# Performance work log

Hardware: AMD Instinct MI355X
Metric: run time of the kernel (lower is better)

The kernel has to match this reference:

```python
import jax, jax.numpy as jnp
import numpy as np

E, B, C_IN, H, W = 4, 32, 64, 64, 64
C_OUT, KH, KW = 128, 3, 3


def setup_inputs() -> dict:
    key = jax.random.key(0)
    k1, k2 = jax.random.split(key)
    features = jax.random.normal(k1, (E, B, C_IN, H, W), dtype=jnp.float32)
    # weight: ensemble + (in, out) + kernel, Glorot-style std = out_channels**-0.5
    weight = jax.random.normal(k2, (E, C_IN, C_OUT, KH, KW), dtype=jnp.float32) * (C_OUT ** -0.5)
    bias = jnp.zeros((E, C_OUT), dtype=jnp.float32)
    return {"features": features, "weight": weight, "bias": bias}


def reference(features, weight, bias):
    # features: (E, B, C_in, H, W); weight: (E, C_in, C_out, KH, KW); bias: (E, C_out)
    # The torch module's unfold+einsum equals a VALID cross-correlation per ensemble member:
    # out[e,b,j,y,x] = sum_{i,A,B} features[e,b,i,y+A,x+B] * weight[e,i,j,A,B]
    def conv_one(x, w):
        k = jnp.transpose(w, (1, 0, 2, 3))  # (C_out, C_in, KH, KW) = OIHW
        return jax.lax.conv_general_dilated(
            x, k, window_strides=(1, 1), padding="VALID",
            dimension_numbers=("NCHW", "OIHW", "NCHW"))

    out = jax.vmap(conv_one)(features, weight)  # (E, B, C_out, H', W')
    out = out + bias[:, None, :, None, None]
    return out
```

## Files before the change

### kernel.cpp

```cpp
#include <hip/hip_runtime.h>

typedef __bf16 bf16x8 __attribute__((ext_vector_type(8)));
typedef __bf16 bf16x2 __attribute__((ext_vector_type(2)));
typedef float  f32x4  __attribute__((ext_vector_type(4)));

#define FT_BYTES 67108864ull

__device__ __forceinline__ void gl2lds16(const void* g, void* l) {
    __builtin_amdgcn_global_load_lds(
        (const __attribute__((address_space(1))) void*)g,
        (__attribute__((address_space(3))) void*)l, 16, 0, 0);
}

__global__ void wt_prep(const float* __restrict__ w, __bf16* __restrict__ wt) {
    int o = blockIdx.x * 256 + threadIdx.x;
    int i = o & 63, j = (o >> 6) & 127, et = o >> 13;
    int tap = et % 9, e = et / 9;
    wt[o] = (__bf16)w[((e * 64 + i) * 128 + j) * 9 + tap];
}

__global__ void ft_prep(const float* __restrict__ f, __bf16* __restrict__ ft) {
    __shared__ float s[64 * 65];
    int eb = blockIdx.z * 32 + blockIdx.y, y = blockIdx.x;
    const float* src = f + (size_t)eb * 262144 + y * 64;
    int t = threadIdx.x;
    for (int r = 0; r < 4; ++r) {
        int f4 = r * 256 + t;
        int i = f4 >> 4, x4 = (f4 & 15) * 4;
        float4 v = *(const float4*)(src + i * 4096 + x4);
        s[i * 65 + x4 + 0] = v.x; s[i * 65 + x4 + 1] = v.y;
        s[i * 65 + x4 + 2] = v.z; s[i * 65 + x4 + 3] = v.w;
    }
    __syncthreads();
    bf16x2* dst = (bf16x2*)(ft + (size_t)(eb * 64 + y) * 4096);
    for (int r = 0; r < 8; ++r) {
        int q = r * 256 + t;
        int x = q >> 5, ih = q & 31;
        bf16x2 pv;
        pv.x = (__bf16)s[(2 * ih + 0) * 65 + x];
        pv.y = (__bf16)s[(2 * ih + 1) * 65 + x];
        dst[q] = pv;
    }
}

__global__ __launch_bounds__(256, 2)
void conv_main(const __bf16* __restrict__ ft, const __bf16* __restrict__ wt,
               const float* __restrict__ bias, float* __restrict__ out) {
    __shared__ __align__(16) __bf16 sA[128 * 64];
    __shared__ __align__(16) __bf16 sB[128 * 64];
    const int e = blockIdx.z, b = blockIdx.y, y0 = blockIdx.x * 2;
    const int eb = e * 32 + b;
    const int t = threadIdx.x, lane = t & 63, w = t >> 6;
    const int wm = w >> 1, wn = w & 1;
    const int q = lane >> 4, rm = lane & 15;

    f32x4 acc[4][4] = {};
    const __bf16* ftb = ft + (size_t)eb * 262144;

    for (int tap = 0; tap < 9; ++tap) {
        const int A = tap / 3, Bt = tap - A * 3;
        __syncthreads();
        const __bf16* wtap = wt + ((size_t)(e * 9 + tap) << 13);
        for (int cc = 0; cc < 4; ++cc) {
            int c = w * 4 + cc;
            int r = c * 8 + (lane >> 3);
            int g = (lane & 7) ^ (r & 7);
            gl2lds16(wtap + r * 64 + g * 8, sA + c * 512);
        }
        const int yA = y0 + A;
        for (int cc = 0; cc < 4; ++cc) {
            int c = w * 4 + cc;
            int p = c * 8 + (lane >> 3);
            int py = p >> 6, px = p & 63;
            int xx = px + Bt; if (xx > 63) xx = 63;
            int g = (lane & 7) ^ (p & 7);
            gl2lds16(ftb + (((yA + py) * 64 + xx) << 6) + g * 8, sB + c * 512);
        }
        __syncthreads();
        for (int kk = 0; kk < 64; kk += 32) {
            const int kg = kk >> 3;
            bf16x8 af[4], bq[4];
            for (int mi = 0; mi < 4; ++mi) {
                int r = wm * 64 + mi * 16 + rm;
                int ch = (kg + q) ^ (r & 7);
                af[mi] = *(const bf16x8*)(sA + r * 64 + ch * 8);
            }
            for (int ni = 0; ni < 4; ++ni) {
                int r = wn * 64 + ni * 16 + rm;
                int ch = (kg + q) ^ (r & 7);
                bq[ni] = *(const bf16x8*)(sB + r * 64 + ch * 8);
            }
            for (int mi = 0; mi < 4; ++mi)
                for (int ni = 0; ni < 4; ++ni)
                    acc[mi][ni] = __builtin_amdgcn_mfma_f32_16x16x32_bf16(
                        af[mi], bq[ni], acc[mi][ni], 0, 0, 0);
        }
    }

    for (int mi = 0; mi < 4; ++mi) {
        for (int ni = 0; ni < 4; ++ni) {
            int p = wn * 64 + ni * 16 + rm;
            int py = p >> 6, px = p & 63;
            if (px >= 62) continue;
            for (int vv = 0; vv < 4; ++vv) {
                int j = wm * 64 + mi * 16 + q * 4 + vv;
                float v = acc[mi][ni][vv] + bias[e * 128 + j];
                out[(((size_t)eb * 128 + j) * 62 + (y0 + py)) * 62 + px] = v;
            }
        }
    }
}

extern "C" void kernel_launch(void* const* d_in, const int* in_sizes, int n_in,
                              void* d_out, int out_size, void* d_ws, size_t ws_size,
                              hipStream_t stream) {
    const float* f    = (const float*)d_in[0];
    const float* wgt  = (const float*)d_in[1];
    const float* bias = (const float*)d_in[2];
    float* out = (float*)d_out;
    __bf16* ftw = (__bf16*)d_ws;
    __bf16* wtw = (__bf16*)((char*)d_ws + FT_BYTES);

    ft_prep<<<dim3(64, 32, 4), 256, 0, stream>>>(f, ftw);
    wt_prep<<<dim3(1152), 256, 0, stream>>>(wgt, wtw);
    conv_main<<<dim3(31, 32, 4), 256, 0, stream>>>(ftw, wtw, bias, out);
}
```

Measured before the change: 422.0 us.

## Stage input halo once in LDS and read weights directly from global

The conv kernel now loads the four input rows (two output rows plus halo) into LDS once, then serves all nine taps from that tile instead of reloading per tap. This removes the per-tap syncs. Weight fragments are read straight from global/L2 per MFMA step rather than being staged in LDS, and occupancy is raised to three blocks per SM. The weight prep kernel is rewritten to read coalesced and scatter its writes. The trade-off is that weight reads now go through the cache hierarchy on every tap and k-step, which may add latency.

```diff
diff --git a/kernel.cpp b/kernel.cpp
--- a/kernel.cpp
+++ b/kernel.cpp
@@ -13,10 +13,12 @@
 }
 
 __global__ void wt_prep(const float* __restrict__ w, __bf16* __restrict__ wt) {
-    int o = blockIdx.x * 256 + threadIdx.x;
-    int i = o & 63, j = (o >> 6) & 127, et = o >> 13;
-    int tap = et % 9, e = et / 9;
-    wt[o] = (__bf16)w[((e * 64 + i) * 128 + j) * 9 + tap];
+    int idx = blockIdx.x * 256 + threadIdx.x;
+    float v = w[idx];
+    int tap = idx % 9, r1 = idx / 9;
+    int j = r1 & 127, r2 = r1 >> 7;
+    int i = r2 & 63, e = r2 >> 6;
+    wt[((e * 9 + tap) * 128 + j) * 64 + i] = (__bf16)v;
 }
 
 __global__ void ft_prep(const float* __restrict__ f, __bf16* __restrict__ ft) {
@@ -43,52 +45,48 @@
     }
 }
 
-__global__ __launch_bounds__(256, 2)
+__global__ __launch_bounds__(256, 3)
 void conv_main(const __bf16* __restrict__ ft, const __bf16* __restrict__ wt,
                const float* __restrict__ bias, float* __restrict__ out) {
-    __shared__ __align__(16) __bf16 sA[128 * 64];
-    __shared__ __align__(16) __bf16 sB[128 * 64];
+    __shared__ __align__(16) __bf16 sB[256 * 64];
     const int e = blockIdx.z, b = blockIdx.y, y0 = blockIdx.x * 2;
     const int eb = e * 32 + b;
     const int t = threadIdx.x, lane = t & 63, w = t >> 6;
     const int wm = w >> 1, wn = w & 1;
     const int q = lane >> 4, rm = lane & 15;
 
+    const __bf16* ftb = ft + (size_t)eb * 262144 + (size_t)y0 * 4096;
+    for (int cc = 0; cc < 8; ++cc) {
+        int C = (cc * 4 + w) * 64 + lane;
+        int r = C >> 3;
+        int g = (lane & 7) ^ (r & 7);
+        gl2lds16(ftb + r * 64 + g * 8, sB + C * 8);
+    }
+    __syncthreads();
+
     f32x4 acc[4][4] = {};
-    const __bf16* ftb = ft + (size_t)eb * 262144;
+    const __bf16* wte = wt + (size_t)e * 9 * 8192;
 
     for (int tap = 0; tap < 9; ++tap) {
         const int A = tap / 3, Bt = tap - A * 3;
-        __syncthreads();
-        const __bf16* wtap = wt + ((size_t)(e * 9 + tap) << 13);
-        for (int cc = 0; cc < 4; ++cc) {
-            int c = w * 4 + cc;
-            int r = c * 8 + (lane >> 3);
-            int g = (lane & 7) ^ (r & 7);
-            gl2lds16(wtap + r * 64 + g * 8, sA + c * 512);
+        const __bf16* wtap = wte + tap * 8192;
+        int rr[4];
+        for (int ni = 0; ni < 4; ++ni) {
+            int n = wn * 64 + ni * 16 + rm;
+            int px = n & 63, py = n >> 6;
+            int xx = px + Bt; if (xx > 63) xx = 63;
+            rr[ni] = (A + py) * 64 + xx;
         }
-        const int yA = y0 + A;
-        for (int cc = 0; cc < 4; ++cc) {
-            int c = w * 4 + cc;
-            int p = c * 8 + (lane >> 3);
-            int py = p >> 6, px = p & 63;
-            int xx = px + Bt; if (xx > 63) xx = 63;
-            int g = (lane & 7) ^ (p & 7);
-            gl2lds16(ftb + (((yA + py) * 64 + xx) << 6) + g * 8, sB + c * 512);
-        }
-        __syncthreads();
-        for (int kk = 0; kk < 64; kk += 32) {
-            const int kg = kk >> 3;
+        for (int kk = 0; kk < 2; ++kk) {
+            const int kg = kk * 4;
             bf16x8 af[4], bq[4];
             for (int mi = 0; mi < 4; ++mi) {
-                int r = wm * 64 + mi * 16 + rm;
-                int ch = (kg + q) ^ (r & 7);
-                af[mi] = *(const bf16x8*)(sA + r * 64 + ch * 8);
+                int j = wm * 64 + mi * 16 + rm;
+                af[mi] = *(const bf16x8*)(wtap + j * 64 + (kg + q) * 8);
             }
             for (int ni = 0; ni < 4; ++ni) {
-                int r = wn * 64 + ni * 16 + rm;
-                int ch = (kg + q) ^ (r & 7);
-                bq[ni] = *(const bf16x8*)(sB + r * 64 + ch * 8);
+                int ch = (kg + q) ^ (rr[ni] & 7);
+                bq[ni] = *(const bf16x8*)(sB + rr[ni] * 64 + ch * 8);
             }
             for (int mi = 0; mi < 4; ++mi)
                 for (int ni = 0; ni < 4; ++ni)
```

Result: slower. 510.1 us (+20.9%).
